# Optimization experiments

Measured on AMD Instinct MI355X. Metric: run time of the kernel, lower is better.

Reference implementation:

```python
import jax, jax.numpy as jnp
import numpy as np

M, D, H, E = 4096, 2048, 2048, 8


def q8(t):
    # Emulate fp8 e4m3 quantize->dequantize (DeepGEMM inputs); scale is all-ones in the source.
    return t.astype(jnp.float8_e4m3fn).astype(jnp.float32)


def setup_inputs() -> dict:
    key = jax.random.key(0)
    k1, k2, k3 = jax.random.split(key, 3)
    x = jax.random.normal(k1, (M, D), dtype=jnp.float32)
    gate_w = jax.random.normal(k2, (E, D), dtype=jnp.float32) * (D ** -0.5)
    gate_b = jnp.zeros((E,), dtype=jnp.float32)
    expert_w = jax.random.normal(k3, (E, H, D), dtype=jnp.float32) * (D ** -0.5)
    return {"x": x, "gate_w": gate_w, "gate_b": gate_b, "expert_w": expert_w}


def reference(x, gate_w, gate_b, expert_w):
    # Gating: softmax over experts. [M, E]
    gate_scores = jax.nn.softmax(x @ gate_w.T + gate_b, axis=-1)
    # fp8 quantize-dequantize of activations and expert weights (rhs_scale == 1).
    x_q = q8(x)                      # [M, D]
    w_q = q8(expert_w)               # [E, H, D]
    # Grouped GEMM (every expert applied to every token), bf16 output like deep_gemm.
    y = jnp.einsum("md,ehd->emh", x_q, w_q).astype(jnp.bfloat16)  # [E, M, H]
    # Weighted combine: sum_e gate[m,e] * y[e,m,h]
    out = jnp.einsum("me,emh->mh", gate_scores, y.astype(jnp.float32))  # [M, H]
    return out
```

## Files before the change

kernel.cpp:

```cpp
#include <hip/hip_runtime.h>
#include <hip/hip_bf16.h>

#define MDIM 4096
#define DDIM 2048
#define HDIM 2048
#define EDIM 8

typedef float v4f __attribute__((ext_vector_type(4)));
typedef int   v4i __attribute__((ext_vector_type(4)));
typedef int   v8i __attribute__((ext_vector_type(8)));

__device__ __forceinline__ void gl2lds16(const void* g, void* l) {
  __builtin_amdgcn_global_load_lds(
      (const __attribute__((address_space(1))) void*)g,
      (__attribute__((address_space(3))) void*)l,
      16, 0, 0);
}

__global__ __launch_bounds__(256) void k_gate_xq(
    const float* __restrict__ x, const float* __restrict__ gw,
    const float* __restrict__ gb, float* __restrict__ gate,
    unsigned char* __restrict__ x8)
{
  const int wid  = threadIdx.x >> 6;
  const int lane = threadIdx.x & 63;
  const int m    = blockIdx.x * 4 + wid;

  const float4* xr = (const float4*)(x + (size_t)m * DDIM);
  unsigned int* qr = (unsigned int*)(x8 + (size_t)m * DDIM);

  float part[EDIM];
#pragma unroll
  for (int e = 0; e < EDIM; ++e) part[e] = 0.f;

#pragma unroll
  for (int it = 0; it < DDIM / 4 / 64; ++it) {
    const int idx = it * 64 + lane;
    const float4 xv = xr[idx];
    int pk = __builtin_amdgcn_cvt_pk_fp8_f32(xv.x, xv.y, 0, false);
    pk = __builtin_amdgcn_cvt_pk_fp8_f32(xv.z, xv.w, pk, true);
    qr[idx] = (unsigned int)pk;
#pragma unroll
    for (int e = 0; e < EDIM; ++e) {
      const float4 wv = ((const float4*)(gw + (size_t)e * DDIM))[idx];
      part[e] += xv.x * wv.x + xv.y * wv.y + xv.z * wv.z + xv.w * wv.w;
    }
  }
#pragma unroll
  for (int e = 0; e < EDIM; ++e) {
#pragma unroll
    for (int off = 32; off > 0; off >>= 1)
      part[e] += __shfl_xor(part[e], off);
  }
  float lg[EDIM];
  float s = 0.f;
#pragma unroll
  for (int e = 0; e < EDIM; ++e) lg[e] = part[e] + gb[e];
  float mx = lg[0];
#pragma unroll
  for (int e = 1; e < EDIM; ++e) mx = fmaxf(mx, lg[e]);
#pragma unroll
  for (int e = 0; e < EDIM; ++e) { lg[e] = expf(lg[e] - mx); s += lg[e]; }
  const float inv = 1.f / s;
  if (lane < EDIM) gate[m * EDIM + lane] = lg[lane] * inv;
}

__global__ void k_wq(const float* __restrict__ w, unsigned char* __restrict__ w8)
{
  const long long n4 = (long long)EDIM * HDIM * DDIM / 4;
  const long long stride = (long long)gridDim.x * blockDim.x;
  for (long long i = (long long)blockIdx.x * blockDim.x + threadIdx.x; i < n4;
       i += stride) {
    const float4 v = ((const float4*)w)[i];
    int pk = __builtin_amdgcn_cvt_pk_fp8_f32(v.x, v.y, 0, false);
    pk = __builtin_amdgcn_cvt_pk_fp8_f32(v.z, v.w, pk, true);
    ((unsigned int*)w8)[i] = (unsigned int)pk;
  }
}

__global__ __launch_bounds__(256, 2) void k_moe_gemm(
    const unsigned char* __restrict__ x8,
    const unsigned char* __restrict__ w8,
    const float* __restrict__ gate,
    float* __restrict__ out)
{
  __shared__ __align__(16) unsigned char sA[2 * 16384];
  __shared__ __align__(16) unsigned char sB[2 * 16384];

  const int tid  = threadIdx.x;
  const int lane = tid & 63;
  const int wid  = tid >> 6;
  const int wm   = wid >> 1;
  const int wn   = wid & 1;

  const int bid   = blockIdx.x;
  const int xcd   = bid & 7;
  const int local = bid >> 3;
  const int tm    = (xcd >> 1) * 8 + (local >> 3);
  const int tn    = (xcd & 1) * 8 + (local & 7);
  const int bm    = tm * 128;
  const int bn    = tn * 128;

  const int lrow = lane & 15;
  const int lk   = lane >> 4;
  const int swz  = (lrow & 7) << 4;
  const int c0   = (lk * 32) ^ swz;
  const int c1   = (lk * 32 + 16) ^ swz;

  const int srow[4] = {(0 * 4096 + tid * 16) >> 7, (1 * 4096 + tid * 16) >> 7,
                       (2 * 4096 + tid * 16) >> 7, (3 * 4096 + tid * 16) >> 7};
  const int scol[4] = {
      ((0 * 4096 + tid * 16) & 127) ^ ((srow[0] & 7) << 4),
      ((1 * 4096 + tid * 16) & 127) ^ ((srow[1] & 7) << 4),
      ((2 * 4096 + tid * 16) & 127) ^ ((srow[2] & 7) << 4),
      ((3 * 4096 + tid * 16) & 127) ^ ((srow[3] & 7) << 4)};

  v4f outacc[4][4];
  v4f acc[4][4];
#pragma unroll
  for (int i = 0; i < 4; ++i)
#pragma unroll
    for (int j = 0; j < 4; ++j) {
      outacc[i][j][0] = 0.f; outacc[i][j][1] = 0.f;
      outacc[i][j][2] = 0.f; outacc[i][j][3] = 0.f;
      acc[i][j][0] = 0.f; acc[i][j][1] = 0.f;
      acc[i][j][2] = 0.f; acc[i][j][3] = 0.f;
    }

  {
#pragma unroll
    for (int i = 0; i < 4; ++i) {
      gl2lds16(x8 + (size_t)(bm + srow[i]) * DDIM + scol[i],
               (void*)(sA + i * 4096 + wid * 1024));
      gl2lds16(w8 + (size_t)(bn + srow[i]) * DDIM + scol[i],
               (void*)(sB + i * 4096 + wid * 1024));
    }
  }
  __syncthreads();

#define MOE_STEP(IT, RB, SB)                                                   \
  {                                                                            \
    const int itn = (IT) + 1;                                                  \
    if (itn < 128) {                                                           \
      const unsigned char* wbe =                                               \
          w8 + (size_t)(itn >> 4) * ((size_t)HDIM * DDIM);                     \
      const int k0n = (itn & 15) * 128;                                        \
      _Pragma("unroll") for (int i = 0; i < 4; ++i) {                          \
        gl2lds16(x8 + (size_t)(bm + srow[i]) * DDIM + k0n + scol[i],           \
                 (void*)(sA + (SB) * 16384 + i * 4096 + wid * 1024));          \
        gl2lds16(wbe + (size_t)(bn + srow[i]) * DDIM + k0n + scol[i],          \
                 (void*)(sB + (SB) * 16384 + i * 4096 + wid * 1024));          \
      }                                                                        \
    }                                                                          \
    const unsigned char* pA = sA + (RB) * 16384;                               \
    const unsigned char* pB = sB + (RB) * 16384;                               \
    v8i av[4];                                                                 \
    _Pragma("unroll") for (int f = 0; f < 4; ++f) {                            \
      const unsigned char* pa = pA + (size_t)(wm * 64 + f * 16 + lrow) * 128;  \
      union { v8i v; v4i h[2]; } u;                                            \
      u.h[0] = *(const v4i*)(pa + c0);                                         \
      u.h[1] = *(const v4i*)(pa + c1);                                         \
      av[f] = u.v;                                                             \
    }                                                                          \
    _Pragma("unroll") for (int j = 0; j < 4; ++j) {                            \
      const unsigned char* pb = pB + (size_t)(wn * 64 + j * 16 + lrow) * 128;  \
      union { v8i v; v4i h[2]; } u;                                            \
      u.h[0] = *(const v4i*)(pb + c0);                                         \
      u.h[1] = *(const v4i*)(pb + c1);                                         \
      const v8i bvj = u.v;                                                     \
      _Pragma("unroll") for (int i = 0; i < 4; ++i)                            \
        acc[i][j] = __builtin_amdgcn_mfma_scale_f32_16x16x128_f8f6f4(          \
            av[i], bvj, acc[i][j], 0 , 0 ,                       \
            0, 127 , 0, 127 );                         \
    }                                                                          \
    if (((IT) & 15) == 15) {                                                   \
      const int e = (IT) >> 4;                                                 \
      _Pragma("unroll") for (int i = 0; i < 4; ++i) {                          \
        float g[4];                                                            \
        _Pragma("unroll") for (int q = 0; q < 4; ++q)                          \
          g[q] =                                                               \
              gate[(size_t)(bm + wm * 64 + i * 16 + lk * 4 + q) * EDIM + e];   \
        _Pragma("unroll") for (int j = 0; j < 4; ++j)                          \
          _Pragma("unroll") for (int q = 0; q < 4; ++q) {                      \
            const float yb = __bfloat162float(__float2bfloat16(acc[i][j][q])); \
            outacc[i][j][q] += g[q] * yb;                                      \
            acc[i][j][q] = 0.f;                                                \
          }                                                                    \
      }                                                                        \
    }                                                                          \
    __syncthreads();                                                           \
  }

  for (int it = 0; it < 128; it += 2) {
    MOE_STEP(it, 0, 1);
    MOE_STEP(it + 1, 1, 0);
  }
#undef MOE_STEP

#pragma unroll
  for (int i = 0; i < 4; ++i)
#pragma unroll
    for (int q = 0; q < 4; ++q) {
      const size_t r = (size_t)(bm + wm * 64 + i * 16 + lk * 4 + q);
      float* orow = out + r * HDIM + bn + wn * 64 + lrow;
#pragma unroll
      for (int j = 0; j < 4; ++j)
        orow[j * 16] = outacc[i][j][q];
    }
}

extern "C" void kernel_launch(void* const* d_in, const int* in_sizes, int n_in,
                              void* d_out, int out_size, void* d_ws, size_t ws_size,
                              hipStream_t stream) {
  (void)in_sizes; (void)n_in; (void)out_size; (void)ws_size;
  const float* x        = (const float*)d_in[0];
  const float* gate_w   = (const float*)d_in[1];
  const float* gate_b   = (const float*)d_in[2];
  const float* expert_w = (const float*)d_in[3];
  float* out = (float*)d_out;

  char* ws = (char*)d_ws;
  float* gate       = (float*)ws;
  unsigned char* x8 = (unsigned char*)(ws + 131072);
  unsigned char* w8 = (unsigned char*)(ws + 131072 + (size_t)MDIM * DDIM);

  hipLaunchKernelGGL(k_gate_xq, dim3(MDIM / 4), dim3(256), 0, stream,
                     x, gate_w, gate_b, gate, x8);
  hipLaunchKernelGGL(k_wq, dim3(4096), dim3(256), 0, stream, expert_w, w8);
  hipLaunchKernelGGL(k_moe_gemm, dim3(512), dim3(256), 0, stream,
                     x8, w8, gate, out);
}
```

Measured before the change: 182.9 us.

## Enlarge GEMM tile to 256x128 with 512 threads and triple-buffered LDS pipeline

Doubles the M tile per block (256 rows, 8 waves, 256 blocks) so each loaded weight tile feeds twice as many rows. Replaces the double buffer plus full __syncthreads with a 3-stage LDS ring that prefetches two steps ahead, using explicit vmcnt waits and s_barrier. Gate values are staged once in LDS, and MFMA sections get raised wave priority. The cost is more LDS per block (about 152KB dynamic), which limits occupancy, plus fragile hand-tuned wait counts.

```diff
diff --git a/kernel.cpp b/kernel.cpp
--- a/kernel.cpp
+++ b/kernel.cpp
@@ -78,14 +78,13 @@
   }
 }
 
-__global__ __launch_bounds__(256, 2) void k_moe_gemm(
+__global__ __launch_bounds__(512, 2) void k_moe_gemm(
     const unsigned char* __restrict__ x8,
     const unsigned char* __restrict__ w8,
     const float* __restrict__ gate,
     float* __restrict__ out)
 {
-  __shared__ __align__(16) unsigned char sA[2 * 16384];
-  __shared__ __align__(16) unsigned char sB[2 * 16384];
+  extern __shared__ unsigned char smem[];
 
   const int tid  = threadIdx.x;
   const int lane = tid & 63;
@@ -96,9 +95,9 @@
   const int bid   = blockIdx.x;
   const int xcd   = bid & 7;
   const int local = bid >> 3;
-  const int tm    = (xcd >> 1) * 8 + (local >> 3);
+  const int tm    = (xcd >> 1) * 4 + (local >> 3);
   const int tn    = (xcd & 1) * 8 + (local & 7);
-  const int bm    = tm * 128;
+  const int bm    = tm * 256;
   const int bn    = tn * 128;
 
   const int lrow = lane & 15;
@@ -107,13 +106,18 @@
   const int c0   = (lk * 32) ^ swz;
   const int c1   = (lk * 32 + 16) ^ swz;
 
-  const int srow[4] = {(0 * 4096 + tid * 16) >> 7, (1 * 4096 + tid * 16) >> 7,
-                       (2 * 4096 + tid * 16) >> 7, (3 * 4096 + tid * 16) >> 7};
-  const int scol[4] = {
-      ((0 * 4096 + tid * 16) & 127) ^ ((srow[0] & 7) << 4),
-      ((1 * 4096 + tid * 16) & 127) ^ ((srow[1] & 7) << 4),
-      ((2 * 4096 + tid * 16) & 127) ^ ((srow[2] & 7) << 4),
-      ((3 * 4096 + tid * 16) & 127) ^ ((srow[3] & 7) << 4)};
+  float* sG = (float*)(smem + 3 * 49152);
+
+  const int strow = tid >> 3;
+  const int stcol = ((tid & 7) * 16) ^ ((strow & 7) << 4);
+  const unsigned char* abase[4];
+  const unsigned char* bbase[2];
+#pragma unroll
+  for (int i = 0; i < 4; ++i)
+    abase[i] = x8 + (size_t)(bm + i * 64 + strow) * DDIM + stcol;
+#pragma unroll
+  for (int i = 0; i < 2; ++i)
+    bbase[i] = w8 + (size_t)(bn + i * 64 + strow) * DDIM + stcol;
 
   v4f outacc[4][4];
   v4f acc[4][4];
@@ -127,75 +131,86 @@
       acc[i][j][2] = 0.f; acc[i][j][3] = 0.f;
     }
 
-  {
-#pragma unroll
-    for (int i = 0; i < 4; ++i) {
-      gl2lds16(x8 + (size_t)(bm + srow[i]) * DDIM + scol[i],
-               (void*)(sA + i * 4096 + wid * 1024));
-      gl2lds16(w8 + (size_t)(bn + srow[i]) * DDIM + scol[i],
-               (void*)(sB + i * 4096 + wid * 1024));
-    }
-  }
-  __syncthreads();
-
-#define MOE_STEP(IT, RB, SB)                                                   \
-  {                                                                            \
-    const int itn = (IT) + 1;                                                  \
-    if (itn < 128) {                                                           \
-      const unsigned char* wbe =                                               \
-          w8 + (size_t)(itn >> 4) * ((size_t)HDIM * DDIM);                     \
-      const int k0n = (itn & 15) * 128;                                        \
-      _Pragma("unroll") for (int i = 0; i < 4; ++i) {                          \
-        gl2lds16(x8 + (size_t)(bm + srow[i]) * DDIM + k0n + scol[i],           \
-                 (void*)(sA + (SB) * 16384 + i * 4096 + wid * 1024));          \
-        gl2lds16(wbe + (size_t)(bn + srow[i]) * DDIM + k0n + scol[i],          \
-                 (void*)(sB + (SB) * 16384 + i * 4096 + wid * 1024));          \
-      }                                                                        \
+#define STAGE(IT, BUF) do {                                                    \
+    const int e_ = (IT) >> 4;                                                  \
+    const int k_ = ((IT) & 15) * 128;                                          \
+    const size_t boff_ = (size_t)e_ * ((size_t)HDIM * DDIM) + k_;              \
+    unsigned char* la_ = smem + (BUF) * 49152;                                 \
+    unsigned char* lb_ = la_ + 32768;                                          \
+    _Pragma("unroll") for (int i = 0; i < 4; ++i)                              \
+      gl2lds16(abase[i] + k_, (void*)(la_ + i * 8192 + wid * 1024));           \
+    _Pragma("unroll") for (int i = 0; i < 2; ++i)                              \
+      gl2lds16(bbase[i] + boff_, (void*)(lb_ + i * 8192 + wid * 1024));        \
+  } while (0)
+
+#define COMP(BUF, T) do {                                                      \
+    const unsigned char* pA_ = smem + (BUF) * 49152 +                          \
+                               (size_t)(wm * 64 + lrow) * 128;                 \
+    const unsigned char* pB_ = smem + (BUF) * 49152 + 32768 +                  \
+                               (size_t)(wn * 64 + lrow) * 128;                 \
+    v8i av_[4];                                                                \
+    _Pragma("unroll") for (int f = 0; f < 4; ++f) {                            \
+      union { v8i v; v4i h[2]; } u_;                                           \
+      u_.h[0] = *(const v4i*)(pA_ + f * 2048 + c0);                            \
+      u_.h[1] = *(const v4i*)(pA_ + f * 2048 + c1);                            \
+      av_[f] = u_.v;                                                           \
     }                                                                          \
-    const unsigned char* pA = sA + (RB) * 16384;                               \
-    const unsigned char* pB = sB + (RB) * 16384;                               \
-    v8i av[4];                                                                 \
-    _Pragma("unroll") for (int f = 0; f < 4; ++f) {                            \
-      const unsigned char* pa = pA + (size_t)(wm * 64 + f * 16 + lrow) * 128;  \
-      union { v8i v; v4i h[2]; } u;                                            \
-      u.h[0] = *(const v4i*)(pa + c0);                                         \
-      u.h[1] = *(const v4i*)(pa + c1);                                         \
-      av[f] = u.v;                                                             \
-    }                                                                          \
+    __builtin_amdgcn_s_setprio(1);                                             \
     _Pragma("unroll") for (int j = 0; j < 4; ++j) {                            \
-      const unsigned char* pb = pB + (size_t)(wn * 64 + j * 16 + lrow) * 128;  \
-      union { v8i v; v4i h[2]; } u;                                            \
-      u.h[0] = *(const v4i*)(pb + c0);                                         \
-      u.h[1] = *(const v4i*)(pb + c1);                                         \
-      const v8i bvj = u.v;                                                     \
+      union { v8i v; v4i h[2]; } u_;                                           \
+      u_.h[0] = *(const v4i*)(pB_ + j * 2048 + c0);                            \
+      u_.h[1] = *(const v4i*)(pB_ + j * 2048 + c1);                            \
+      const v8i bv_ = u_.v;                                                    \
       _Pragma("unroll") for (int i = 0; i < 4; ++i)                            \
         acc[i][j] = __builtin_amdgcn_mfma_scale_f32_16x16x128_f8f6f4(          \
-            av[i], bvj, acc[i][j], 0 , 0 ,                       \
+            av_[i], bv_, acc[i][j], 0 , 0 ,                      \
             0, 127 , 0, 127 );                         \
     }                                                                          \
-    if (((IT) & 15) == 15) {                                                   \
-      const int e = (IT) >> 4;                                                 \
-      _Pragma("unroll") for (int i = 0; i < 4; ++i) {                          \
-        float g[4];                                                            \
-        _Pragma("unroll") for (int q = 0; q < 4; ++q)                          \
-          g[q] =                                                               \
-              gate[(size_t)(bm + wm * 64 + i * 16 + lk * 4 + q) * EDIM + e];   \
-        _Pragma("unroll") for (int j = 0; j < 4; ++j)                          \
-          _Pragma("unroll") for (int q = 0; q < 4; ++q) {                      \
-            const float yb = __bfloat162float(__float2bfloat16(acc[i][j][q])); \
-            outacc[i][j][q] += g[q] * yb;                                      \
+    __builtin_amdgcn_s_setprio(0);                                             \
+    if (((T) & 15) == 15) {                                                    \
+      const int e_ = (T) >> 4;                                                 \
+      _Pragma("unroll") for (int i = 0; i < 4; ++i)                            \
+        _Pragma("unroll") for (int q = 0; q < 4; ++q) {                        \
+          const float g_ = sG[(wm * 64 + i * 16 + lk * 4 + q) * 8 + e_];       \
+          _Pragma("unroll") for (int j = 0; j < 4; ++j) {                      \
+            const float yb_ =                                                  \
+                __bfloat162float(__float2bfloat16(acc[i][j][q]));              \
+            outacc[i][j][q] += g_ * yb_;                                       \
             acc[i][j][q] = 0.f;                                                \
           }                                                                    \
-      }                                                                        \
+        }                                                                      \
     }                                                                          \
-    __syncthreads();                                                           \
-  }
-
-  for (int it = 0; it < 128; it += 2) {
-    MOE_STEP(it, 0, 1);
-    MOE_STEP(it + 1, 1, 0);
-  }
-#undef MOE_STEP
+  } while (0)
+
+#define STEP(T, BUF, SBUF, WAIT) do {                                          \
+    if ((T) + 2 < 128) STAGE((T) + 2, (SBUF));                                 \
+    asm volatile("s_waitcnt vmcnt(" #WAIT ")" ::: "memory");                   \
+    __builtin_amdgcn_s_barrier();                                              \
+    __builtin_amdgcn_sched_barrier(0);                                         \
+    COMP((BUF), (T));                                                          \
+    __builtin_amdgcn_sched_barrier(0);                                         \
+    __builtin_amdgcn_s_barrier();                                              \
+  } while (0)
+
+  {
+    const float4 gv = *(const float4*)(gate + (size_t)bm * EDIM + tid * 4);
+    ((float4*)sG)[tid] = gv;
+  }
+  STAGE(0, 0);
+  STAGE(1, 1);
+  __syncthreads();
+
+  for (int t0 = 0; t0 < 126; t0 += 3) {
+    STEP(t0 + 0, 0, 2, 12);
+    STEP(t0 + 1, 1, 0, 12);
+    STEP(t0 + 2, 2, 1, 12);
+  }
+  STEP(126, 0, 2, 6);
+  STEP(127, 1, 2, 0);
+
+#undef STEP
+#undef COMP
+#undef STAGE
 
 #pragma unroll
   for (int i = 0; i < 4; ++i)
@@ -227,6 +242,6 @@
   hipLaunchKernelGGL(k_gate_xq, dim3(MDIM / 4), dim3(256), 0, stream,
                      x, gate_w, gate_b, gate, x8);
   hipLaunchKernelGGL(k_wq, dim3(4096), dim3(256), 0, stream, expert_w, w8);
-  hipLaunchKernelGGL(k_moe_gemm, dim3(512), dim3(256), 0, stream,
-                     x8, w8, gate, out);
-}
+  hipLaunchKernelGGL(k_moe_gemm, dim3(256), dim3(512),
+                     3 * 49152 + 8192, stream, x8, w8, gate, out);
+}
```

After: 191.3 us. +4.6%, slower.
